# Kernel tuning notes

Measured on AMD Instinct MI355X. Metric: run time of the kernel, lower is better.

Reference implementation:

```python
import jax, jax.numpy as jnp
import numpy as np

B, C, O, H, W = 8, 64, 64, 128, 128


def conv3x3(x, w, b):
    # x: [B,Cin,H,W], w: [Cout,Cin,3,3], stride 1, padding 1
    y = jax.lax.conv_general_dilated(
        x, w, window_strides=(1, 1), padding=((1, 1), (1, 1)),
        dimension_numbers=("NCHW", "OIHW", "NCHW"))
    return y + b[None, :, None, None]


def setup_inputs() -> dict:
    key = jax.random.key(0)
    ks = jax.random.split(key, 6)
    fan = C * 9
    x = jax.random.normal(ks[0], (B, C, H, W), dtype=jnp.float32)
    w_main = jax.random.normal(ks[1], (O, C, 3, 3), dtype=jnp.float32) / np.sqrt(fan)
    # small offset weights keep sampled locations near the regular grid (realistic post-training regime)
    w_offset = jax.random.normal(ks[2], (18, C, 3, 3), dtype=jnp.float32) * 0.05 / np.sqrt(fan)
    b_offset = jnp.zeros((18,), dtype=jnp.float32)
    w_mask = jax.random.normal(ks[3], (9, C, 3, 3), dtype=jnp.float32) / np.sqrt(fan)
    b_mask = jnp.zeros((9,), dtype=jnp.float32)
    return {"x": x, "w_main": w_main, "w_offset": w_offset,
            "b_offset": b_offset, "w_mask": w_mask, "b_mask": b_mask}


def deform_conv2d(x, w_main, offset, mask):
    # torchvision.ops.deform_conv2d: kernel 3x3, stride 1, pad 1, dilation 1, no bias
    Bb, Cc, Hh, Ww = x.shape
    Oo = w_main.shape[0]
    off = offset.reshape(Bb, 9, 2, Hh, Ww)
    dy, dx = off[:, :, 0], off[:, :, 1]            # [B,9,H,W]; pairs ordered (y,x), k row-major
    k = jnp.arange(9)
    kh = (k // 3 - 1).astype(x.dtype)              # kernel row offset in {-1,0,1}
    kw = (k % 3 - 1).astype(x.dtype)
    iy = jnp.arange(Hh, dtype=x.dtype)
    ix = jnp.arange(Ww, dtype=x.dtype)
    # sampling positions p = p0 + p_k + delta_p
    py = dy + iy[None, None, :, None] + kh[None, :, None, None]
    px = dx + ix[None, None, None, :] + kw[None, :, None, None]

    y0 = jnp.floor(py)
    x0 = jnp.floor(px)
    ly = py - y0
    lx = px - x0
    y0i = y0.astype(jnp.int32)
    x0i = x0.astype(jnp.int32)
    y1i = y0i + 1
    x1i = x0i + 1

    bidx = jnp.arange(Bb)[:, None, None, None]

    def corner(yi, xi, wgt):
        # zero-padding semantics: out-of-bounds neighbors contribute 0
        valid = (yi >= 0) & (yi < Hh) & (xi >= 0) & (xi < Ww)
        v = x[bidx, :, jnp.clip(yi, 0, Hh - 1), jnp.clip(xi, 0, Ww - 1)]  # [B,9,H,W,C]
        return v * (wgt * valid)[..., None]

    samp = (corner(y0i, x0i, (1 - ly) * (1 - lx))
            + corner(y0i, x1i, (1 - ly) * lx)
            + corner(y1i, x0i, ly * (1 - lx))
            + corner(y1i, x1i, ly * lx))
    samp = samp * mask[..., None]                  # modulation mask (dcn v2)
    # contract sampled patches with weights: [B,9,H,W,C] x [O,C,9] -> [B,O,H,W]
    return jnp.einsum("bkhwc,ock->bohw", samp, w_main.reshape(Oo, Cc, 9))


def reference(x, w_main, w_offset, b_offset, w_mask, b_mask):
    offset = conv3x3(x, w_offset, b_offset)                 # [B,18,H,W]
    mask = jax.nn.sigmoid(conv3x3(x, w_mask, b_mask))       # [B,9,H,W]
    return deform_conv2d(x, w_main, offset, mask)
```

## Files before the change

### kernel.cpp

```cpp
#include <hip/hip_runtime.h>
#include <math.h>

#define BB 8
#define CC 64
#define OO 64
#define HH 128
#define WW 128
#define HW (HH*WW)
#define NPIX (BB*HW)

typedef __bf16 bf16x8 __attribute__((ext_vector_type(8)));
typedef float floatx4 __attribute__((ext_vector_type(4)));
typedef unsigned short ushort_t;

#define XT_BYTES  16777216
#define OM_BYTES  14680064
#define WT_BYTES  73728

__device__ __forceinline__ unsigned short f2b(float f) {
    unsigned u = __float_as_uint(f);
    u += 0x7fffu + ((u >> 16) & 1u);
    return (unsigned short)(u >> 16);
}

__device__ __forceinline__ void unpack8(uint4 q, float* f) {
    f[0] = __uint_as_float(q.x << 16); f[1] = __uint_as_float(q.x & 0xffff0000u);
    f[2] = __uint_as_float(q.y << 16); f[3] = __uint_as_float(q.y & 0xffff0000u);
    f[4] = __uint_as_float(q.z << 16); f[5] = __uint_as_float(q.z & 0xffff0000u);
    f[6] = __uint_as_float(q.w << 16); f[7] = __uint_as_float(q.w & 0xffff0000u);
}

__global__ __launch_bounds__(256) void transpose_kernel(
    const float* __restrict__ x, ushort_t* __restrict__ xt)
{
    __shared__ float tile[64][33];
    int bh = blockIdx.x;
    int w0 = blockIdx.y * 32;
    int b  = bh >> 7;
    int h  = bh & 127;
    int t  = threadIdx.x;
    int tx = t & 31;
    int ty = t >> 5;

    #pragma unroll
    for (int j = 0; j < 8; ++j) {
        int c = ty * 8 + j;
        tile[c][tx] = x[(((size_t)(b*CC + c))*HH + h)*WW + (w0 + tx)];
    }
    __syncthreads();
    #pragma unroll
    for (int j = 0; j < 4; ++j) {
        int w  = ty + 8*j;
        int cp = tx;
        unsigned u = (unsigned)f2b(tile[2*cp][w]) |
                     ((unsigned)f2b(tile[2*cp+1][w]) << 16);
        *(unsigned*)(xt + (((size_t)(b*HH + h))*WW + (w0 + w))*CC + 2*cp) = u;
    }
}

__global__ __launch_bounds__(256) void repack_kernel(
    const float* __restrict__ wm, const float* __restrict__ woff,
    const float* __restrict__ wmask, ushort_t* __restrict__ wt,
    ushort_t* __restrict__ wb)
{
    int i = blockIdx.x * 256 + threadIdx.x;
    if (i < 36864) {
        int o = i / 576, k = i % 576, tap = k >> 6, c = k & 63;
        wt[i] = f2b(wm[o*576 + c*9 + tap]);
    }
    int j = i - 36864;
    if (j >= 0 && j < 18432) {
        int o = j / 576, k = j % 576, tap = k >> 6, c = k & 63;
        float v = 0.f;
        if (o < 18)      v = woff[o*576 + c*9 + tap];
        else if (o < 27) v = wmask[(o-18)*576 + c*9 + tap];
        wb[j] = f2b(v);
    }
}

__global__ __launch_bounds__(256) void conv27_kernel(
    const ushort_t* __restrict__ xt, const ushort_t* __restrict__ wb,
    const float* __restrict__ boff, const float* __restrict__ bmsk,
    float* __restrict__ om)
{
    __shared__ ushort_t win[18*18*72];
    int bid = blockIdx.x;
    int b  = bid >> 6;
    int th = (bid >> 3) & 7;
    int tw = bid & 7;
    int h0 = th * 16, w0 = tw * 16;
    int t = threadIdx.x;

    for (int idx = t; idx < 18*18*8; idx += 256) {
        int r   = idx / 144;
        int rem = idx - r*144;
        int col = rem >> 3;
        int ch  = (rem & 7) << 3;
        int y = h0 + r - 1, x = w0 + col - 1;
        uint4 val = make_uint4(0,0,0,0);
        if ((unsigned)y < (unsigned)HH && (unsigned)x < (unsigned)WW)
            val = *(const uint4*)(xt + ((((size_t)b*HH + y)*WW + x) << 6) + ch);
        *(uint4*)(win + (r*18 + col)*72 + ch) = val;
    }
    __syncthreads();

    int lane = t & 63, wv = t >> 6;
    int n = lane & 15, quad = lane >> 4;
    const ushort_t* wb0 = wb + n*576;
    const ushort_t* wb1 = wb + (16 + n)*576;

    floatx4 acc0[4], acc1[4];
    #pragma unroll
    for (int mt = 0; mt < 4; ++mt) {
        acc0[mt] = (floatx4){0.f,0.f,0.f,0.f};
        acc1[mt] = (floatx4){0.f,0.f,0.f,0.f};
    }

    #pragma unroll
    for (int s = 0; s < 18; ++s) {
        int tap  = s >> 1;
        int tr   = tap / 3, tc = tap % 3;
        int coff = (s & 1)*32 + quad*8;
        int kk = tap*64 + coff;
        bf16x8 b0 = *(const bf16x8*)(wb0 + kk);
        bf16x8 b1 = *(const bf16x8*)(wb1 + kk);
        #pragma unroll
        for (int mt = 0; mt < 4; ++mt) {
            int ty = wv*4 + mt;
            bf16x8 a = *(const bf16x8*)(win + ((ty + tr)*18 + (n + tc))*72 + coff);
            acc0[mt] = __builtin_amdgcn_mfma_f32_16x16x32_bf16(a, b0, acc0[mt], 0, 0, 0);
            acc1[mt] = __builtin_amdgcn_mfma_f32_16x16x32_bf16(a, b1, acc1[mt], 0, 0, 0);
        }
    }

    #pragma unroll
    for (int mt = 0; mt < 4; ++mt) {
        int ty = wv*4 + mt;
        #pragma unroll
        for (int r = 0; r < 4; ++r) {
            int tx = quad*4 + r;
            size_t p = ((size_t)(b*HH + h0 + ty))*WW + (w0 + tx);
            float* dst = om + p*28;
            dst[n] = acc0[mt][r] + boff[n];
            int o1 = 16 + n;
            if (o1 < 18) {
                dst[o1] = acc1[mt][r] + boff[o1];
            } else if (o1 < 27) {
                float z = acc1[mt][r] + bmsk[o1 - 18];
                dst[o1] = 1.f / (1.f + expf(-z));
            } else if (o1 == 27) {
                dst[27] = 0.f;
            }
        }
    }
}

__global__ __launch_bounds__(256) void deform_kernel(
    const ushort_t* __restrict__ xt, const float* __restrict__ om,
    const ushort_t* __restrict__ wt, float* __restrict__ out)
{
    __shared__ ushort_t samp[2*64*72];

    int t = threadIdx.x;
    int lane = t & 63, wv = t >> 6;
    int bid = blockIdx.x;
    int b  = bid >> 8;
    int th = (bid >> 4) & 15;
    int tw = bid & 15;
    int h0 = th * 8, w0 = tw * 8;

    int pa = t >> 2, cg = t & 3;
    int ph = pa >> 3, pw = pa & 7;
    int h_a = h0 + ph, w_a = w0 + pw;
    const float* omp = om + (((size_t)(b*HH + h_a))*WW + w_a) * 28;
    const ushort_t* xbase = xt + ((size_t)b << 20);

    int n = lane & 15, quad = lane >> 4;
    floatx4 acc[4];
    #pragma unroll
    for (int i = 0; i < 4; ++i) acc[i] = (floatx4){0.f,0.f,0.f,0.f};
    const ushort_t* wrow = wt + (wv*16 + n)*576;

    float dy = omp[0], dx = omp[1], m = omp[18];

    for (int k = 0; k < 9; ++k) {
        ushort_t* sb = samp + (k & 1) * (64*72);

        float dy_n = 0.f, dx_n = 0.f, m_n = 0.f;
        if (k < 8) { dy_n = omp[2*k + 2]; dx_n = omp[2*k + 3]; m_n = omp[19 + k]; }

        int kr = k / 3, kc = k - kr*3;
        float py = (float)(h_a + kr - 1) + dy;
        float px = (float)(w_a + kc - 1) + dx;
        float y0f = floorf(py), x0f = floorf(px);
        float ly = py - y0f, lx = px - x0f;
        int y0 = (int)y0f, x0 = (int)x0f, y1 = y0 + 1, x1 = x0 + 1;
        float vy0 = ((unsigned)y0 < (unsigned)HH) ? 1.f : 0.f;
        float vy1 = ((unsigned)y1 < (unsigned)HH) ? 1.f : 0.f;
        float vx0 = ((unsigned)x0 < (unsigned)WW) ? 1.f : 0.f;
        float vx1 = ((unsigned)x1 < (unsigned)WW) ? 1.f : 0.f;

        float cw[4] = { (1.f-ly)*(1.f-lx)*vy0*vx0*m,
                        (1.f-ly)*lx      *vy0*vx1*m,
                        ly*(1.f-lx)      *vy1*vx0*m,
                        ly*lx            *vy1*vx1*m };
        int ys[4] = { y0, y0, y1, y1 };
        int xs[4] = { x0, x1, x0, x1 };

        dy = dy_n; dx = dx_n; m = m_n;

        float v[16];
        #pragma unroll
        for (int i = 0; i < 16; ++i) v[i] = 0.f;

        #pragma unroll
        for (int cn = 0; cn < 4; ++cn) {
            int yc = min(max(ys[cn], 0), HH-1);
            int xc = min(max(xs[cn], 0), WW-1);
            const uint4* cp = (const uint4*)(xbase + (((yc << 7) + xc) << 6) + cg*16);
            uint4 q0 = cp[0], q1 = cp[1];
            float f[16];
            unpack8(q0, f); unpack8(q1, f + 8);
            float wg = cw[cn];
            #pragma unroll
            for (int j = 0; j < 16; ++j) v[j] += wg * f[j];
        }

        {
            unsigned uu[8];
            #pragma unroll
            for (int j = 0; j < 8; ++j)
                uu[j] = (unsigned)f2b(v[2*j]) | ((unsigned)f2b(v[2*j+1]) << 16);
            uint4* dst = (uint4*)(sb + pa*72 + cg*16);
            dst[0] = make_uint4(uu[0], uu[1], uu[2], uu[3]);
            dst[1] = make_uint4(uu[4], uu[5], uu[6], uu[7]);
        }
        __syncthreads();

        #pragma unroll
        for (int half = 0; half < 2; ++half) {
            bf16x8 bfrag = *(const bf16x8*)(wrow + k*64 + half*32 + quad*8);
            #pragma unroll
            for (int mt = 0; mt < 4; ++mt) {
                bf16x8 afrag = *(const bf16x8*)(sb + (mt*16 + n)*72 + half*32 + quad*8);
                acc[mt] = __builtin_amdgcn_mfma_f32_16x16x32_bf16(afrag, bfrag, acc[mt], 0, 0, 0);
            }
        }
        __syncthreads();
    }

    float* op = out + ((size_t)b*OO + (wv*16 + n))*HW;
    #pragma unroll
    for (int mt = 0; mt < 4; ++mt) {
        int row = h0 + mt*2 + (quad >> 1);
        int col = w0 + (quad & 1)*4;
        float4 st = make_float4(acc[mt][0], acc[mt][1], acc[mt][2], acc[mt][3]);
        *(float4*)(op + row*WW + col) = st;
    }
}

extern "C" void kernel_launch(void* const* d_in, const int* in_sizes, int n_in,
                              void* d_out, int out_size, void* d_ws, size_t ws_size,
                              hipStream_t stream)
{
    const float* x      = (const float*)d_in[0];
    const float* w_main = (const float*)d_in[1];
    const float* w_off  = (const float*)d_in[2];
    const float* b_off  = (const float*)d_in[3];
    const float* w_msk  = (const float*)d_in[4];
    const float* b_msk  = (const float*)d_in[5];
    float* out = (float*)d_out;

    unsigned char* ws = (unsigned char*)d_ws;
    ushort_t* xt = (ushort_t*)ws;
    float*    om = (float*)(ws + XT_BYTES);
    ushort_t* wt = (ushort_t*)(ws + XT_BYTES + OM_BYTES);
    ushort_t* wb = (ushort_t*)(ws + XT_BYTES + OM_BYTES + WT_BYTES);

    dim3 tgrid(BB*HH, WW/32);
    transpose_kernel<<<tgrid, 256, 0, stream>>>(x, xt);

    repack_kernel<<<(36864 + 18432 + 255)/256, 256, 0, stream>>>(
        w_main, w_off, w_msk, wt, wb);

    conv27_kernel<<<NPIX/256, 256, 0, stream>>>(xt, wb, b_off, b_msk, om);

    deform_kernel<<<NPIX/64, 256, 0, stream>>>(xt, om, wt, out);
}
```

Baseline: 162.9 us.

## Fuse offset/mask conv into deform kernel with shared halo window

```diff
diff --git a/kernel.cpp b/kernel.cpp
--- a/kernel.cpp
+++ b/kernel.cpp
@@ -11,23 +11,16 @@
 
 typedef __bf16 bf16x8 __attribute__((ext_vector_type(8)));
 typedef float floatx4 __attribute__((ext_vector_type(4)));
+typedef float f32x2  __attribute__((ext_vector_type(2)));
 typedef unsigned short ushort_t;
 
 #define XT_BYTES  16777216
-#define OM_BYTES  14680064
 #define WT_BYTES  73728
 
 __device__ __forceinline__ unsigned short f2b(float f) {
     unsigned u = __float_as_uint(f);
     u += 0x7fffu + ((u >> 16) & 1u);
     return (unsigned short)(u >> 16);
-}
-
-__device__ __forceinline__ void unpack8(uint4 q, float* f) {
-    f[0] = __uint_as_float(q.x << 16); f[1] = __uint_as_float(q.x & 0xffff0000u);
-    f[2] = __uint_as_float(q.y << 16); f[3] = __uint_as_float(q.y & 0xffff0000u);
-    f[4] = __uint_as_float(q.z << 16); f[5] = __uint_as_float(q.z & 0xffff0000u);
-    f[6] = __uint_as_float(q.w << 16); f[7] = __uint_as_float(q.w & 0xffff0000u);
 }
 
 __global__ __launch_bounds__(256) void transpose_kernel(
@@ -78,88 +71,17 @@
     }
 }
 
-__global__ __launch_bounds__(256) void conv27_kernel(
+#define WR 14
+#define WSTRIDE 72
+
+__global__ __launch_bounds__(256) void fused_kernel(
     const ushort_t* __restrict__ xt, const ushort_t* __restrict__ wb,
     const float* __restrict__ boff, const float* __restrict__ bmsk,
-    float* __restrict__ om)
-{
-    __shared__ ushort_t win[18*18*72];
-    int bid = blockIdx.x;
-    int b  = bid >> 6;
-    int th = (bid >> 3) & 7;
-    int tw = bid & 7;
-    int h0 = th * 16, w0 = tw * 16;
-    int t = threadIdx.x;
-
-    for (int idx = t; idx < 18*18*8; idx += 256) {
-        int r   = idx / 144;
-        int rem = idx - r*144;
-        int col = rem >> 3;
-        int ch  = (rem & 7) << 3;
-        int y = h0 + r - 1, x = w0 + col - 1;
-        uint4 val = make_uint4(0,0,0,0);
-        if ((unsigned)y < (unsigned)HH && (unsigned)x < (unsigned)WW)
-            val = *(const uint4*)(xt + ((((size_t)b*HH + y)*WW + x) << 6) + ch);
-        *(uint4*)(win + (r*18 + col)*72 + ch) = val;
-    }
-    __syncthreads();
-
-    int lane = t & 63, wv = t >> 6;
-    int n = lane & 15, quad = lane >> 4;
-    const ushort_t* wb0 = wb + n*576;
-    const ushort_t* wb1 = wb + (16 + n)*576;
-
-    floatx4 acc0[4], acc1[4];
-    #pragma unroll
-    for (int mt = 0; mt < 4; ++mt) {
-        acc0[mt] = (floatx4){0.f,0.f,0.f,0.f};
-        acc1[mt] = (floatx4){0.f,0.f,0.f,0.f};
-    }
-
-    #pragma unroll
-    for (int s = 0; s < 18; ++s) {
-        int tap  = s >> 1;
-        int tr   = tap / 3, tc = tap % 3;
-        int coff = (s & 1)*32 + quad*8;
-        int kk = tap*64 + coff;
-        bf16x8 b0 = *(const bf16x8*)(wb0 + kk);
-        bf16x8 b1 = *(const bf16x8*)(wb1 + kk);
-        #pragma unroll
-        for (int mt = 0; mt < 4; ++mt) {
-            int ty = wv*4 + mt;
-            bf16x8 a = *(const bf16x8*)(win + ((ty + tr)*18 + (n + tc))*72 + coff);
-            acc0[mt] = __builtin_amdgcn_mfma_f32_16x16x32_bf16(a, b0, acc0[mt], 0, 0, 0);
-            acc1[mt] = __builtin_amdgcn_mfma_f32_16x16x32_bf16(a, b1, acc1[mt], 0, 0, 0);
-        }
-    }
-
-    #pragma unroll
-    for (int mt = 0; mt < 4; ++mt) {
-        int ty = wv*4 + mt;
-        #pragma unroll
-        for (int r = 0; r < 4; ++r) {
-            int tx = quad*4 + r;
-            size_t p = ((size_t)(b*HH + h0 + ty))*WW + (w0 + tx);
-            float* dst = om + p*28;
-            dst[n] = acc0[mt][r] + boff[n];
-            int o1 = 16 + n;
-            if (o1 < 18) {
-                dst[o1] = acc1[mt][r] + boff[o1];
-            } else if (o1 < 27) {
-                float z = acc1[mt][r] + bmsk[o1 - 18];
-                dst[o1] = 1.f / (1.f + expf(-z));
-            } else if (o1 == 27) {
-                dst[27] = 0.f;
-            }
-        }
-    }
-}
-
-__global__ __launch_bounds__(256) void deform_kernel(
-    const ushort_t* __restrict__ xt, const float* __restrict__ om,
     const ushort_t* __restrict__ wt, float* __restrict__ out)
 {
+    __shared__ ushort_t win[WR*WR*WSTRIDE];
     __shared__ ushort_t samp[2*64*72];
+    __shared__ float    om_lds[64*28];
 
     int t = threadIdx.x;
     int lane = t & 63, wv = t >> 6;
@@ -168,28 +90,75 @@
     int th = (bid >> 4) & 15;
     int tw = bid & 15;
     int h0 = th * 8, w0 = tw * 8;
+    const ushort_t* xbase = xt + ((size_t)b << 20);
+
+    for (int idx = t; idx < WR*WR*8; idx += 256) {
+        int r   = idx / (WR*8);
+        int rem = idx - r*(WR*8);
+        int col = rem >> 3;
+        int ch  = (rem & 7) << 3;
+        int y = h0 + r - 3, x = w0 + col - 3;
+        uint4 val = make_uint4(0,0,0,0);
+        if ((unsigned)y < (unsigned)HH && (unsigned)x < (unsigned)WW)
+            val = *(const uint4*)(xbase + (((y << 7) + x) << 6) + ch);
+        *(uint4*)(win + (r*WR + col)*WSTRIDE + ch) = val;
+    }
+    __syncthreads();
+
+    int n = lane & 15, quad = lane >> 4;
+
+    {
+        const ushort_t* wb0 = wb + n*576;
+        const ushort_t* wb1 = wb + (16 + n)*576;
+        floatx4 acc0 = {0.f,0.f,0.f,0.f}, acc1 = {0.f,0.f,0.f,0.f};
+        int trow = wv*2 + (n >> 3);
+        int tcol = n & 7;
+
+        #pragma unroll
+        for (int s = 0; s < 18; ++s) {
+            int tap  = s >> 1;
+            int tr   = tap / 3, tc = tap % 3;
+            int coff = (s & 1)*32 + quad*8;
+            int kk = tap*64 + coff;
+            bf16x8 b0 = *(const bf16x8*)(wb0 + kk);
+            bf16x8 b1 = *(const bf16x8*)(wb1 + kk);
+            bf16x8 a = *(const bf16x8*)(win +
+                ((trow + tr + 2)*WR + (tcol + tc + 2))*WSTRIDE + coff);
+            acc0 = __builtin_amdgcn_mfma_f32_16x16x32_bf16(a, b0, acc0, 0, 0, 0);
+            acc1 = __builtin_amdgcn_mfma_f32_16x16x32_bf16(a, b1, acc1, 0, 0, 0);
+        }
+
+        #pragma unroll
+        for (int r = 0; r < 4; ++r) {
+            int p = wv*16 + quad*4 + r;
+            float* dst = om_lds + p*28;
+            dst[n] = acc0[r] + boff[n];
+            int o1 = 16 + n;
+            if (o1 < 18) {
+                dst[o1] = acc1[r] + boff[o1];
+            } else if (o1 < 27) {
+                float z = acc1[r] + bmsk[o1 - 18];
+                dst[o1] = 1.f / (1.f + expf(-z));
+            }
+        }
+    }
+    __syncthreads();
 
     int pa = t >> 2, cg = t & 3;
     int ph = pa >> 3, pw = pa & 7;
     int h_a = h0 + ph, w_a = w0 + pw;
-    const float* omp = om + (((size_t)(b*HH + h_a))*WW + w_a) * 28;
-    const ushort_t* xbase = xt + ((size_t)b << 20);
-
-    int n = lane & 15, quad = lane >> 4;
+    const float* omp = om_lds + pa*28;
+
     floatx4 acc[4];
     #pragma unroll
     for (int i = 0; i < 4; ++i) acc[i] = (floatx4){0.f,0.f,0.f,0.f};
     const ushort_t* wrow = wt + (wv*16 + n)*576;
 
-    float dy = omp[0], dx = omp[1], m = omp[18];
-
     for (int k = 0; k < 9; ++k) {
         ushort_t* sb = samp + (k & 1) * (64*72);
 
-        float dy_n = 0.f, dx_n = 0.f, m_n = 0.f;
-        if (k < 8) { dy_n = omp[2*k + 2]; dx_n = omp[2*k + 3]; m_n = omp[19 + k]; }
-
         int kr = k / 3, kc = k - kr*3;
+        float dy = omp[2*k], dx = omp[2*k + 1], m = omp[18 + k];
         float py = (float)(h_a + kr - 1) + dy;
         float px = (float)(w_a + kc - 1) + dx;
         float y0f = floorf(py), x0f = floorf(px);
@@ -207,30 +176,39 @@
         int ys[4] = { y0, y0, y1, y1 };
         int xs[4] = { x0, x1, x0, x1 };
 
-        dy = dy_n; dx = dx_n; m = m_n;
-
-        float v[16];
-        #pragma unroll
-        for (int i = 0; i < 16; ++i) v[i] = 0.f;
+        f32x2 v2[8];
+        #pragma unroll
+        for (int i = 0; i < 8; ++i) v2[i] = (f32x2){0.f, 0.f};
 
         #pragma unroll
         for (int cn = 0; cn < 4; ++cn) {
             int yc = min(max(ys[cn], 0), HH-1);
             int xc = min(max(xs[cn], 0), WW-1);
-            const uint4* cp = (const uint4*)(xbase + (((yc << 7) + xc) << 6) + cg*16);
-            uint4 q0 = cp[0], q1 = cp[1];
-            float f[16];
-            unpack8(q0, f); unpack8(q1, f + 8);
+            int wy = yc - h0 + 3, wx = xc - w0 + 3;
+            uint4 q0, q1;
+            if ((unsigned)wy < (unsigned)WR && (unsigned)wx < (unsigned)WR) {
+                const uint4* cp = (const uint4*)(win + (wy*WR + wx)*WSTRIDE + cg*16);
+                q0 = cp[0]; q1 = cp[1];
+            } else {
+                const uint4* cp = (const uint4*)(xbase + (((yc << 7) + xc) << 6) + cg*16);
+                q0 = cp[0]; q1 = cp[1];
+            }
+            unsigned d[8] = { q0.x, q0.y, q0.z, q0.w, q1.x, q1.y, q1.z, q1.w };
             float wg = cw[cn];
             #pragma unroll
-            for (int j = 0; j < 16; ++j) v[j] += wg * f[j];
+            for (int j = 0; j < 8; ++j) {
+                f32x2 e;
+                e.x = __uint_as_float(d[j] << 16);
+                e.y = __uint_as_float(d[j] & 0xffff0000u);
+                v2[j] += e * wg;
+            }
         }
 
         {
             unsigned uu[8];
             #pragma unroll
             for (int j = 0; j < 8; ++j)
-                uu[j] = (unsigned)f2b(v[2*j]) | ((unsigned)f2b(v[2*j+1]) << 16);
+                uu[j] = (unsigned)f2b(v2[j].x) | ((unsigned)f2b(v2[j].y) << 16);
             uint4* dst = (uint4*)(sb + pa*72 + cg*16);
             dst[0] = make_uint4(uu[0], uu[1], uu[2], uu[3]);
             dst[1] = make_uint4(uu[4], uu[5], uu[6], uu[7]);
@@ -273,9 +251,8 @@
 
     unsigned char* ws = (unsigned char*)d_ws;
     ushort_t* xt = (ushort_t*)ws;
-    float*    om = (float*)(ws + XT_BYTES);
-    ushort_t* wt = (ushort_t*)(ws + XT_BYTES + OM_BYTES);
-    ushort_t* wb = (ushort_t*)(ws + XT_BYTES + OM_BYTES + WT_BYTES);
+    ushort_t* wt = (ushort_t*)(ws + XT_BYTES);
+    ushort_t* wb = (ushort_t*)(ws + XT_BYTES + WT_BYTES);
 
     dim3 tgrid(BB*HH, WW/32);
     transpose_kernel<<<tgrid, 256, 0, stream>>>(x, xt);
@@ -283,7 +260,5 @@
     repack_kernel<<<(36864 + 18432 + 255)/256, 256, 0, stream>>>(
         w_main, w_off, w_msk, wt, wb);
 
-    conv27_kernel<<<NPIX/256, 256, 0, stream>>>(xt, wb, b_off, b_msk, om);
-
-    deform_kernel<<<NPIX/64, 256, 0, stream>>>(xt, om, wt, out);
-}
+    fused_kernel<<<NPIX/64, 256, 0, stream>>>(xt, wb, b_off, b_msk, wt, out);
+}
```

New measurement: 190.9 us. 17.2% more time.
